# Performance work log

Measured on AMD Instinct MI355X. Metric: run time of the kernel, lower is better.

The kernel has to match this reference:

```python
import jax, jax.numpy as jnp
import numpy as np

N, E, F, H = 8192, 131072, 128, 128
K = N // 2  # pooling ratio = 0.5


def setup_inputs():
    key = jax.random.key(0)
    ks = jax.random.split(key, 16)
    g = lambda i, shape, s: jax.random.normal(ks[i], shape, jnp.float32) * s
    w = 0.1
    return {
        "nodes": g(0, (N, F), 1.0),
        "edges": jax.random.randint(ks[1], (2, E), 0, N, dtype=jnp.int32),
        "batch": jnp.zeros((N,), jnp.int32),
        "w1": g(2, (F, H), w), "b1": jnp.zeros((H,), jnp.float32),
        "w2": g(3, (H, H), w), "b2": jnp.zeros((H,), jnp.float32),
        "w3": g(4, (H, H), w), "b3": jnp.zeros((H,), jnp.float32),
        "w4": g(5, (H, H), w), "b4": jnp.zeros((H,), jnp.float32),
        "w5": g(6, (H, F), w), "b5": jnp.zeros((F,), jnp.float32),
        "wq": g(7, (H, H), w), "bq": jnp.zeros((H,), jnp.float32),
        "att": g(8, (2 * H,), w),
        "lw1": g(9, (H, 1), w), "lb1": jnp.zeros((1,), jnp.float32),
        "lw2": g(10, (H, 1), w), "lw3": g(11, (H, 1), w),
    }


def reference(nodes, edges, batch, w1, b1, w2, b2, w3, b3, w4, b4, w5, b5,
              wq, bq, att, lw1, lb1, lw2, lw3):
    n = nodes.shape[0]
    src, dst = edges[0], edges[1]
    loop = jnp.arange(n, dtype=src.dtype)
    srcl = jnp.concatenate([src, loop])  # edges + self loops
    dstl = jnp.concatenate([dst, loop])
    deg = jax.ops.segment_sum(jnp.ones(srcl.shape[0], nodes.dtype), dstl, n)
    dis = jax.lax.rsqrt(jnp.maximum(deg, 1.0))
    norm = dis[srcl] * dis[dstl]  # GCN symmetric normalization

    def gcn(x, w, b):
        return jax.ops.segment_sum((x @ w)[srcl] * norm[:, None], dstl, n) + b

    h = jnp.tanh(gcn(nodes, w1, b1))
    h = jnp.tanh(gcn(h, w2, b2))

    # ---- ASAP pooling ----
    h_src = h[srcl]
    # cluster query: max over 1-hop neighborhood, then linear
    xq = jax.ops.segment_max(h_src, dstl, n) @ wq + bq
    # edge attention score, softmax per destination (cluster)
    e = jax.nn.leaky_relu(jnp.concatenate([xq[dstl], h_src], axis=-1) @ att, 0.2)
    ee = jnp.exp(e - jax.ops.segment_max(e, dstl, n)[dstl])
    alpha = ee / jax.ops.segment_sum(ee, dstl, n)[dstl]
    cx = jax.ops.segment_sum(h_src * alpha[:, None], dstl, n)  # cluster reps [N,H]
    # LEConv fitness score (out_dim = 1)
    aggr = jax.ops.segment_sum((cx @ lw2)[dstl] - (cx @ lw3)[srcl], dstl, n)
    fit = jax.nn.sigmoid((cx @ lw1 + lb1 + aggr)[:, 0])
    fitk, perm = jax.lax.top_k(fit, K)
    xp = cx[perm] * fitk[:, None]  # pooled node features [K,H]
    # dense assignment matrix S [N,K]: S[i, j] = alpha(i -> perm[j])
    inv = jnp.full((n,), -1, jnp.int32).at[perm].set(jnp.arange(K, dtype=jnp.int32))
    col = inv[dstl]
    valid = col >= 0
    S = jnp.zeros((n, K), nodes.dtype).at[
        srcl, jnp.where(valid, col, 0)].add(jnp.where(valid, alpha, 0.0))
    # dense adjacency (with self loops) and coarsened adjacency Ac = S^T A S
    A = jnp.zeros((n, n), nodes.dtype).at[srcl, dstl].add(1.0)
    Ac = S.T @ (A @ S)  # [K,K]

    # ---- autoencoder reconstruction via bmm with S ----
    x_out = S @ xp               # [N,H]
    adj_out = S @ (Ac @ S.T)     # [N,N]

    x2 = jnp.tanh(gcn(x_out, w3, b3))
    x2 = jnp.tanh(gcn(x2, w4, b4))
    x2 = gcn(x2, w5, b5)
    return x2, adj_out[None]
```

## Files before the change

### kernel.cpp

```cpp
#include <hip/hip_runtime.h>
#include <math.h>

#define NN 8192
#define EE 131072
#define ELn 139264
#define HH 128
#define KK 4096

__device__ __forceinline__ int esrc(const int* __restrict__ edges, int e){ return e < EE ? edges[e] : e - EE; }
__device__ __forceinline__ int edst(const int* __restrict__ edges, int e){ return e < EE ? edges[EE + e] : e - EE; }

__global__ void k_count(const int* __restrict__ edges, int* __restrict__ indeg, int* __restrict__ outdeg){
  int e = blockIdx.x*blockDim.x + threadIdx.x;
  if (e < ELn){
    atomicAdd(&indeg[edst(edges,e)], 1);
    atomicAdd(&outdeg[esrc(edges,e)], 1);
  }
}

__global__ void k_dis(const int* __restrict__ deg, float* __restrict__ dis){
  int v = blockIdx.x*blockDim.x + threadIdx.x;
  if (v < NN){ float d = (float)deg[v]; d = d < 1.0f ? 1.0f : d; dis[v] = 1.0f/sqrtf(d); }
}

template<int IPT>
__global__ __launch_bounds__(1024) void k_scan(const int* __restrict__ cnt, int* __restrict__ rowptr, int* __restrict__ cur){
  __shared__ int part[1024];
  int tid = threadIdx.x;
  int base = tid*IPT;
  int loc[IPT]; int s=0;
  #pragma unroll
  for (int i=0;i<IPT;i++) loc[i]=cnt[base+i];
  #pragma unroll
  for (int i=0;i<IPT;i++){ int t=loc[i]; loc[i]=s; s+=t; }
  part[tid]=s;
  __syncthreads();
  for (int off=1; off<1024; off<<=1){
    int v = (tid>=off)? part[tid-off] : 0;
    __syncthreads();
    part[tid]+=v;
    __syncthreads();
  }
  int cb = part[tid]-s;
  #pragma unroll
  for (int i=0;i<IPT;i++){ int r=cb+loc[i]; rowptr[base+i]=r; cur[base+i]=r; }
  if (tid==1023) rowptr[1024*IPT]=part[1023];
}

__global__ void k_fill_dst(const int* __restrict__ edges, int* __restrict__ cur,
                           int* __restrict__ delist, int* __restrict__ desrc){
  int e = blockIdx.x*blockDim.x + threadIdx.x;
  if (e < ELn){
    int v = edst(edges,e);
    int pos = atomicAdd(&cur[v],1);
    delist[pos] = e;
    desrc[pos]  = esrc(edges,e);
  }
}
__global__ void k_fill_src(const int* __restrict__ edges, int* __restrict__ cur, int* __restrict__ esdst){
  int e = blockIdx.x*blockDim.x + threadIdx.x;
  if (e < ELn){
    int u = esrc(edges,e);
    int pos = atomicAdd(&cur[u],1);
    esdst[pos] = edst(edges,e);
  }
}

template<int TANH>
__global__ __launch_bounds__(256) void k_layer(const float* __restrict__ x,
    const int* __restrict__ desrc, const int* __restrict__ drowptr,
    const float* __restrict__ dis, const float* __restrict__ W,
    const float* __restrict__ bias, float* __restrict__ out){
  __shared__ float agg[8][HH];
  int tid = threadIdx.x;
  int r0 = blockIdx.x*8;
  int wv = tid>>6, lane = tid&63;
  for (int rr=wv; rr<8; rr+=4){
    int v = r0+rr;
    int beg = drowptr[v], end = drowptr[v+1];
    float ax=0.f, ay=0.f;
    for (int i=beg;i<end;++i){
      int u = desrc[i];
      float du = dis[u];
      float2 xv = *(const float2*)&x[(size_t)u*HH + lane*2];
      ax += du*xv.x; ay += du*xv.y;
    }
    float dv = dis[v];
    *(float2*)&agg[rr][lane*2] = make_float2(ax*dv, ay*dv);
  }
  __syncthreads();
  int c = tid&127, h = tid>>7;
  float a0=0,a1=0,a2=0,a3=0;
  #pragma unroll 4
  for (int k=0;k<HH;++k){
    float wv_ = W[k*HH+c];
    a0 += agg[h*4+0][k]*wv_;
    a1 += agg[h*4+1][k]*wv_;
    a2 += agg[h*4+2][k]*wv_;
    a3 += agg[h*4+3][k]*wv_;
  }
  float b = bias[c];
  float r[4]={a0+b,a1+b,a2+b,a3+b};
  #pragma unroll
  for (int j=0;j<4;j++){
    float v = r[j];
    if (TANH) v = tanhf(v);
    out[(size_t)(r0+h*4+j)*HH + c] = v;
  }
}

__global__ __launch_bounds__(256) void k_gemm8(const float* __restrict__ x, const float* __restrict__ W,
     const float* __restrict__ bias, float* __restrict__ y){
  __shared__ float xl[8*HH];
  int tid = threadIdx.x;
  int r0 = blockIdx.x*8;
  {
    int row = tid>>5, col = (tid&31)*4;
    *(float4*)&xl[row*HH+col] = *(const float4*)&x[(size_t)(r0+row)*HH+col];
  }
  __syncthreads();
  int c = tid & 127, h = tid>>7;
  float acc0=0,acc1=0,acc2=0,acc3=0;
  const float* xr = &xl[h*4*HH];
  #pragma unroll 8
  for (int k=0;k<HH;++k){
    float wv = W[k*HH+c];
    acc0 += xr[k]*wv;
    acc1 += xr[HH+k]*wv;
    acc2 += xr[2*HH+k]*wv;
    acc3 += xr[3*HH+k]*wv;
  }
  float b = bias[c];
  y[(size_t)(r0+h*4+0)*HH + c] = acc0+b;
  y[(size_t)(r0+h*4+1)*HH + c] = acc1+b;
  y[(size_t)(r0+h*4+2)*HH + c] = acc2+b;
  y[(size_t)(r0+h*4+3)*HH + c] = acc3+b;
}

__global__ void k_segmax(const float* __restrict__ h, const int* __restrict__ desrc,
    const int* __restrict__ drowptr, float* __restrict__ out){
  int v = blockIdx.x, f = threadIdx.x;
  int beg = drowptr[v], end = drowptr[v+1];
  float m = -3.4e38f;
  for (int i=beg;i<end;++i){
    int u = desrc[i];
    m = fmaxf(m, h[(size_t)u*HH+f]);
  }
  out[(size_t)v*HH+f] = m;
}

__global__ void k_aqah(const float* __restrict__ xq, const float* __restrict__ h,
                       const float* __restrict__ att, float* __restrict__ aq, float* __restrict__ ah){
  int v = blockIdx.x, t = threadIdx.x;
  float a1 = xq[(size_t)v*HH+t]*att[t];
  float a2 = h[(size_t)v*HH+t]*att[HH+t];
  #pragma unroll
  for (int off=32; off; off>>=1){ a1 += __shfl_down(a1,off); a2 += __shfl_down(a2,off); }
  __shared__ float s1[2], s2[2];
  if ((t&63)==0){ s1[t>>6]=a1; s2[t>>6]=a2; }
  __syncthreads();
  if (t==0){ aq[v]=s1[0]+s1[1]; ah[v]=s2[0]+s2[1]; }
}

__global__ __launch_bounds__(256) void k_alpha(const int* __restrict__ delist, const int* __restrict__ desrc,
    const int* __restrict__ drowptr, const float* __restrict__ aq, const float* __restrict__ ah,
    float* __restrict__ alpha){
  int v = blockIdx.x*4 + (threadIdx.x>>6);
  int lane = threadIdx.x & 63;
  int beg = drowptr[v], end = drowptr[v+1];
  float aqv = aq[v];
  float m = -3.4e38f;
  for (int i=beg+lane; i<end; i+=64){
    float s = aqv + ah[desrc[i]];
    s = s > 0.0f ? s : 0.2f*s;
    m = fmaxf(m, s);
  }
  #pragma unroll
  for (int off=32; off; off>>=1) m = fmaxf(m, __shfl_xor(m, off));
  float den = 0.0f;
  for (int i=beg+lane; i<end; i+=64){
    float s = aqv + ah[desrc[i]];
    s = s > 0.0f ? s : 0.2f*s;
    den += expf(s - m);
  }
  #pragma unroll
  for (int off=32; off; off>>=1) den += __shfl_xor(den, off);
  float inv = 1.0f/den;
  for (int i=beg+lane; i<end; i+=64){
    float s = aqv + ah[desrc[i]];
    s = s > 0.0f ? s : 0.2f*s;
    alpha[delist[i]] = expf(s - m)*inv;
  }
}

__global__ void k_cx(const float* __restrict__ h, const int* __restrict__ delist,
    const int* __restrict__ desrc, const int* __restrict__ drowptr,
    const float* __restrict__ alpha, float* __restrict__ cx){
  int v = blockIdx.x, f = threadIdx.x;
  int beg = drowptr[v], end = drowptr[v+1];
  float acc = 0.0f;
  for (int i=beg;i<end;++i){
    acc += alpha[delist[i]]*h[(size_t)desrc[i]*HH+f];
  }
  cx[(size_t)v*HH+f] = acc;
}

__global__ void k_le(const float* __restrict__ cx, const float* __restrict__ lw1,
                     const float* __restrict__ lw2, const float* __restrict__ lw3,
                     float* __restrict__ l1, float* __restrict__ l2, float* __restrict__ l3){
  int v = blockIdx.x, t = threadIdx.x;
  float cv = cx[(size_t)v*HH+t];
  float a = cv*lw1[t], b = cv*lw2[t], c = cv*lw3[t];
  #pragma unroll
  for (int off=32; off; off>>=1){ a += __shfl_down(a,off); b += __shfl_down(b,off); c += __shfl_down(c,off); }
  __shared__ float sa[2], sb[2], sc[2];
  if ((t&63)==0){ sa[t>>6]=a; sb[t>>6]=b; sc[t>>6]=c; }
  __syncthreads();
  if (t==0){ l1[v]=sa[0]+sa[1]; l2[v]=sb[0]+sb[1]; l3[v]=sc[0]+sc[1]; }
}

__global__ __launch_bounds__(256) void k_fit(const int* __restrict__ desrc, const int* __restrict__ drowptr,
    const float* __restrict__ l1, const float* __restrict__ l2, const float* __restrict__ l3,
    const float* __restrict__ lb1, float* __restrict__ fit){
  int v = blockIdx.x*4 + (threadIdx.x>>6);
  int lane = threadIdx.x & 63;
  int beg = drowptr[v], end = drowptr[v+1];
  float s = 0.0f;
  for (int i=beg+lane;i<end;i+=64) s += l3[desrc[i]];
  #pragma unroll
  for (int off=32; off; off>>=1) s += __shfl_xor(s, off);
  if (lane==0){
    float degf = (float)(end-beg);
    float x = l1[v] + lb1[0] + degf*l2[v] - s;
    fit[v] = 1.0f/(1.0f+expf(-x));
  }
}

__global__ __launch_bounds__(1024) void k_topk(const float* __restrict__ fit, int* __restrict__ perm,
                        float* __restrict__ fitk, int* __restrict__ inv){
  __shared__ unsigned long long keys[NN];
  int tid = threadIdx.x;
  for (int i=tid;i<NN;i+=1024){
    unsigned u = __float_as_uint(fit[i]);
    unsigned mono = (u>>31) ? ~u : (u|0x80000000u);
    keys[i] = ((unsigned long long)(~mono)<<32) | (unsigned)i;
    inv[i] = -1;
  }
  __syncthreads();
  for (int k=2;k<=NN;k<<=1)
    for (int j=k>>1;j>0;j>>=1){
      for (int t=tid;t<NN;t+=1024){
        int ixj = t^j;
        if (ixj > t){
          bool up = ((t&k)==0);
          unsigned long long a = keys[t], b = keys[ixj];
          if (up ? (a>b) : (a<b)){ keys[t]=b; keys[ixj]=a; }
        }
      }
      __syncthreads();
    }
  for (int i=tid;i<KK;i+=1024){
    int idx = (int)(keys[i] & 0xffffffffu);
    perm[i]=idx; fitk[i]=fit[idx]; inv[idx]=i;
  }
}

__global__ void k_xp(const float* __restrict__ cx, const int* __restrict__ perm,
                     const float* __restrict__ fitk, float* __restrict__ xp){
  int j = blockIdx.x, f = threadIdx.x;
  xp[(size_t)j*HH+f] = cx[(size_t)perm[j]*HH+f]*fitk[j];
}

__global__ void k_scnt(const int* __restrict__ edges, const int* __restrict__ inv, int* __restrict__ scnt){
  int e = blockIdx.x*blockDim.x + threadIdx.x;
  if (e < ELn && inv[edst(edges,e)] >= 0) atomicAdd(&scnt[esrc(edges,e)],1);
}

__global__ void k_fill_s(const int* __restrict__ edges, const int* __restrict__ inv,
                         const float* __restrict__ alpha, int* __restrict__ scur,
                         int2* __restrict__ spair, int* __restrict__ srow_of){
  int e = blockIdx.x*blockDim.x + threadIdx.x;
  if (e < ELn){
    int j = inv[edst(edges,e)];
    if (j >= 0){
      int u = esrc(edges,e);
      int pos = atomicAdd(&scur[u],1);
      spair[pos] = make_int2(j, __float_as_int(alpha[e]));
      srow_of[pos] = u;
    }
  }
}

__global__ void k_col_cnt(const int2* __restrict__ spair, const int* __restrict__ srowptr, int* __restrict__ ccnt){
  int i = blockIdx.x*blockDim.x + threadIdx.x;
  if (i < srowptr[NN]) atomicAdd(&ccnt[spair[i].x], 1);
}
__global__ void k_col_fill(const int2* __restrict__ spair, const int* __restrict__ srow_of,
                           const int* __restrict__ srowptr, int* __restrict__ ccur,
                           int* __restrict__ colu, float* __restrict__ cval){
  int i = blockIdx.x*blockDim.x + threadIdx.x;
  if (i < srowptr[NN]){
    int2 p = spair[i];
    int pos = atomicAdd(&ccur[p.x], 1);
    colu[pos] = srow_of[i];
    cval[pos] = __int_as_float(p.y);
  }
}

__global__ void k_xout(const float* __restrict__ xp, const int* __restrict__ srowptr,
                       const int2* __restrict__ spair, float* __restrict__ xout){
  int u = blockIdx.x, f = threadIdx.x;
  int beg = srowptr[u], end = srowptr[u+1];
  float acc = 0.0f;
  for (int i=beg;i<end;++i){
    int2 p = spair[i];
    acc += __int_as_float(p.y)*xp[(size_t)p.x*HH+f];
  }
  xout[(size_t)u*HH+f] = acc;
}

#define ACCAP 2048
__global__ __launch_bounds__(256) void k_ac2(const int* __restrict__ cptr, const int* __restrict__ colu,
     const float* __restrict__ cval, const int* __restrict__ esptr, const int* __restrict__ esdst,
     const int* __restrict__ srowptr, const int2* __restrict__ spair, float* __restrict__ Ac){
  __shared__ float row[KK];
  __shared__ int   lv[ACCAP];
  __shared__ float lval[ACCAP];
  int tid = threadIdx.x;
  int p = blockIdx.x;
  for (int i=tid;i<KK;i+=256) row[i]=0.0f;
  int cb = cptr[p], ce = cptr[p+1];
  int base = 0;
  int j = cb;
  while (true){
    while (j < ce){
      int u = colu[j]; float val = cval[j];
      int eb = esptr[u], d = esptr[u+1]-eb;
      if (base + d > ACCAP) break;
      for (int t=tid; t<d; t+=256){ lv[base+t]=esdst[eb+t]; lval[base+t]=val; }
      base += d; ++j;
    }
    __syncthreads();
    for (int i=tid;i<base;i+=256){
      int v = lv[i]; float a = lval[i];
      int sb = srowptr[v], se = srowptr[v+1];
      for (int k=sb;k<se;++k){
        int2 q = spair[k];
        atomicAdd(&row[q.x], a*__int_as_float(q.y));
      }
    }
    __syncthreads();
    base = 0;
    if (j >= ce) break;
  }
  for (int i=tid;i<KK;i+=256) Ac[(size_t)p*KK+i] = row[i];
}

__global__ __launch_bounds__(1024) void k_adj(const float* __restrict__ Ac, const int* __restrict__ srowptr,
      const int2* __restrict__ spair, float* __restrict__ adj){
  __shared__ float U[8*KK];
  int tid = threadIdx.x;
  int u0 = blockIdx.x*8;
  #pragma unroll
  for (int g=0; g<8; ++g){
    int beg = srowptr[u0+g], end = srowptr[u0+g+1];
    float ux=0.f, uy=0.f, uz=0.f, uw=0.f;
    for (int i=beg;i<end;++i){
      int2 pr = spair[i];
      float a = __int_as_float(pr.y);
      float4 av = *(const float4*)(Ac + (size_t)pr.x*KK + 4*tid);
      ux += a*av.x; uy += a*av.y; uz += a*av.z; uw += a*av.w;
    }
    *(float4*)&U[g*KK + 4*tid] = make_float4(ux,uy,uz,uw);
  }
  __syncthreads();
  for (int wb=0; wb<NN; wb+=1024){
    int w = wb + tid;
    int beg = srowptr[w], end = srowptr[w+1];
    float acc[8];
    #pragma unroll
    for (int g=0;g<8;g++) acc[g]=0.f;
    for (int i=beg;i<end;++i){
      int2 p = spair[i];
      float b = __int_as_float(p.y);
      int q = p.x;
      #pragma unroll
      for (int g=0;g<8;g++) acc[g] += b*U[g*KK+q];
    }
    #pragma unroll
    for (int g=0;g<8;g++)
      __builtin_nontemporal_store(acc[g], &adj[(size_t)(u0+g)*NN + w]);
  }
}

extern "C" void kernel_launch(void* const* d_in, const int* in_sizes, int n_in,
                              void* d_out, int out_size, void* d_ws, size_t ws_size,
                              hipStream_t stream){
  const float* nodes = (const float*)d_in[0];
  const int*   edges = (const int*)d_in[1];
  const float* w1=(const float*)d_in[3];  const float* b1=(const float*)d_in[4];
  const float* w2=(const float*)d_in[5];  const float* b2=(const float*)d_in[6];
  const float* w3=(const float*)d_in[7];  const float* b3=(const float*)d_in[8];
  const float* w4=(const float*)d_in[9];  const float* b4=(const float*)d_in[10];
  const float* w5=(const float*)d_in[11]; const float* b5=(const float*)d_in[12];
  const float* wq=(const float*)d_in[13]; const float* bq=(const float*)d_in[14];
  const float* att=(const float*)d_in[15];
  const float* lw1=(const float*)d_in[16]; const float* lb1=(const float*)d_in[17];
  const float* lw2=(const float*)d_in[18]; const float* lw3=(const float*)d_in[19];

  char* ws = (char*)d_ws;
  size_t off = 0;
  auto take = [&](size_t bytes)->char*{
    char* p = ws + off;
    off = (off + bytes + 255) & ~(size_t)255;
    return p;
  };
  int*   deg     = (int*)  take((size_t)NN*4);
  float* dis     = (float*)take((size_t)NN*4);
  int*   drowptr = (int*)  take((size_t)(NN+1)*4);
  int*   dcur    = (int*)  take((size_t)NN*4);
  int*   delist  = (int*)  take((size_t)ELn*4);
  float* alpha   = (float*)take((size_t)ELn*4);
  float* aq      = (float*)take((size_t)NN*4);
  float* ah      = (float*)take((size_t)NN*4);
  float* l1      = (float*)take((size_t)NN*4);
  float* l2      = (float*)take((size_t)NN*4);
  float* l3      = (float*)take((size_t)NN*4);
  float* fit     = (float*)take((size_t)NN*4);
  int*   perm    = (int*)  take((size_t)KK*4);
  float* fitk    = (float*)take((size_t)KK*4);
  int*   inv     = (int*)  take((size_t)NN*4);
  int*   scnt    = (int*)  take((size_t)NN*4);
  int*   srowptr = (int*)  take((size_t)(NN+1)*4);
  int*   scur    = (int*)  take((size_t)NN*4);
  int2*  spair   = (int2*) take((size_t)ELn*8);
  int*   ecnt    = (int*)  take((size_t)NN*4);
  int*   esptr   = (int*)  take((size_t)(NN+1)*4);
  int*   ecur    = (int*)  take((size_t)NN*4);
  int*   ccnt    = (int*)  take((size_t)KK*4);
  int*   cptr    = (int*)  take((size_t)(KK+1)*4);
  int*   ccur    = (int*)  take((size_t)KK*4);
  float* Ac      = (float*)take((size_t)KK*KK*4);
  (void)ws_size; (void)in_sizes; (void)n_in; (void)out_size;

  float* out_x2 = (float*)d_out;
  float* adj    = (float*)d_out + (size_t)NN*HH;
  float* BB = adj + 0*(size_t)NN*HH;
  float* BC = adj + 1*(size_t)NN*HH;
  float* BD = adj + 2*(size_t)NN*HH;
  float* BE = adj + 3*(size_t)NN*HH;
  float* BF = adj + 4*(size_t)NN*HH;
  float* BG = adj + 5*(size_t)NN*HH;
  float* xp = adj + 6*(size_t)NN*HH;
  char*  sc2 = (char*)(adj + 7*(size_t)NN*HH);
  int*   desrc   = (int*)  sc2;                       sc2 += (size_t)ELn*4;
  int*   esdst   = (int*)  sc2;                       sc2 += (size_t)ELn*4;
  int*   srow_of = (int*)  sc2;                       sc2 += (size_t)ELn*4;
  int*   colu    = (int*)  sc2;                       sc2 += (size_t)ELn*4;
  float* cval    = (float*)sc2;                       sc2 += (size_t)ELn*4;

  const int EB = ELn/256;

  hipMemsetAsync(deg, 0, (size_t)NN*4, stream);
  hipMemsetAsync(ecnt, 0, (size_t)NN*4, stream);
  k_count<<<EB,256,0,stream>>>(edges,deg,ecnt);
  k_dis<<<NN/256,256,0,stream>>>(deg,dis);
  k_scan<8><<<1,1024,0,stream>>>(deg,drowptr,dcur);
  k_fill_dst<<<EB,256,0,stream>>>(edges,dcur,delist,desrc);
  k_scan<8><<<1,1024,0,stream>>>(ecnt,esptr,ecur);
  k_fill_src<<<EB,256,0,stream>>>(edges,ecur,esdst);

  k_layer<1><<<NN/8,256,0,stream>>>(nodes,desrc,drowptr,dis,w1,b1,BB);
  k_layer<1><<<NN/8,256,0,stream>>>(BB,desrc,drowptr,dis,w2,b2,BC);

  k_segmax<<<NN,128,0,stream>>>(BC,desrc,drowptr,BD);
  k_gemm8<<<NN/8,256,0,stream>>>(BD,wq,bq,BE);
  k_aqah<<<NN,128,0,stream>>>(BE,BC,att,aq,ah);
  k_alpha<<<NN/4,256,0,stream>>>(delist,desrc,drowptr,aq,ah,alpha);
  k_cx<<<NN,128,0,stream>>>(BC,delist,desrc,drowptr,alpha,BF);
  k_le<<<NN,128,0,stream>>>(BF,lw1,lw2,lw3,l1,l2,l3);
  k_fit<<<NN/4,256,0,stream>>>(desrc,drowptr,l1,l2,l3,lb1,fit);
  k_topk<<<1,1024,0,stream>>>(fit,perm,fitk,inv);
  k_xp<<<KK,128,0,stream>>>(BF,perm,fitk,xp);

  hipMemsetAsync(scnt, 0, (size_t)NN*4, stream);
  k_scnt<<<EB,256,0,stream>>>(edges,inv,scnt);
  k_scan<8><<<1,1024,0,stream>>>(scnt,srowptr,scur);
  k_fill_s<<<EB,256,0,stream>>>(edges,inv,alpha,scur,spair,srow_of);
  hipMemsetAsync(ccnt, 0, (size_t)KK*4, stream);
  k_col_cnt<<<EB,256,0,stream>>>(spair,srowptr,ccnt);
  k_scan<4><<<1,1024,0,stream>>>(ccnt,cptr,ccur);
  k_col_fill<<<EB,256,0,stream>>>(spair,srow_of,srowptr,ccur,colu,cval);

  k_xout<<<NN,128,0,stream>>>(xp,srowptr,spair,BG);
  k_layer<1><<<NN/8,256,0,stream>>>(BG,desrc,drowptr,dis,w3,b3,BB);
  k_layer<1><<<NN/8,256,0,stream>>>(BB,desrc,drowptr,dis,w4,b4,BD);
  k_layer<0><<<NN/8,256,0,stream>>>(BD,desrc,drowptr,dis,w5,b5,out_x2);

  k_ac2<<<KK,256,0,stream>>>(cptr,colu,cval,esptr,esdst,srowptr,spair,Ac);
  k_adj<<<NN/8,1024,0,stream>>>(Ac,srowptr,spair,adj);
}
```

Baseline: 1.118 ms.

## Fuse graph-build and pooling kernels, replace bitonic top-k with histogram radix select

Several kernels are merged: the two scans run in one two-block launch, the dst and src CSR fills share one pass, segmax+wq gemm+attention dot are fused into k_pool, the ah dot is folded into the second GCN layer, and the LEConv projections are fused into the cx aggregation. The single-block 8192-element bitonic top-k is replaced with a 16-bit histogram select plus a small bitonic sort over tie bins only. The perm/xp arrays are removed, so xout reads cx*fit directly. k_adj processes two rows at a time for more memory-level parallelism, and the memsets are merged into one. This cuts launch count and serial single-block sorting, at the cost of an extra index array and tie-ordering logic whose slot assignment must match top_k.

```diff
diff --git a/kernel.cpp b/kernel.cpp
--- a/kernel.cpp
+++ b/kernel.cpp
@@ -6,6 +6,7 @@
 #define ELn 139264
 #define HH 128
 #define KK 4096
+#define NBIN 65536
 
 __device__ __forceinline__ int esrc(const int* __restrict__ edges, int e){ return e < EE ? edges[e] : e - EE; }
 __device__ __forceinline__ int edst(const int* __restrict__ edges, int e){ return e < EE ? edges[EE + e] : e - EE; }
@@ -24,7 +25,7 @@
 }
 
 template<int IPT>
-__global__ __launch_bounds__(1024) void k_scan(const int* __restrict__ cnt, int* __restrict__ rowptr, int* __restrict__ cur){
+__device__ __forceinline__ void scan_body(const int* __restrict__ cnt, int* __restrict__ rowptr, int* __restrict__ cur){
   __shared__ int part[1024];
   int tid = threadIdx.x;
   int base = tid*IPT;
@@ -46,36 +47,41 @@
   for (int i=0;i<IPT;i++){ int r=cb+loc[i]; rowptr[base+i]=r; cur[base+i]=r; }
   if (tid==1023) rowptr[1024*IPT]=part[1023];
 }
-
-__global__ void k_fill_dst(const int* __restrict__ edges, int* __restrict__ cur,
-                           int* __restrict__ delist, int* __restrict__ desrc){
+template<int IPT>
+__global__ __launch_bounds__(1024) void k_scan(const int* __restrict__ cnt, int* __restrict__ rowptr, int* __restrict__ cur){
+  scan_body<IPT>(cnt, rowptr, cur);
+}
+__global__ __launch_bounds__(1024) void k_scan2(const int* __restrict__ c0, int* __restrict__ r0, int* __restrict__ u0,
+                                                const int* __restrict__ c1, int* __restrict__ r1, int* __restrict__ u1){
+  if (blockIdx.x==0) scan_body<8>(c0,r0,u0);
+  else               scan_body<8>(c1,r1,u1);
+}
+
+__global__ void k_fill_both(const int* __restrict__ edges, int* __restrict__ dcur, int* __restrict__ ecur,
+                            int* __restrict__ delist, int* __restrict__ desrc, int* __restrict__ esdst){
   int e = blockIdx.x*blockDim.x + threadIdx.x;
   if (e < ELn){
-    int v = edst(edges,e);
-    int pos = atomicAdd(&cur[v],1);
+    int v = edst(edges,e), u = esrc(edges,e);
+    int pos = atomicAdd(&dcur[v],1);
     delist[pos] = e;
-    desrc[pos]  = esrc(edges,e);
-  }
-}
-__global__ void k_fill_src(const int* __restrict__ edges, int* __restrict__ cur, int* __restrict__ esdst){
-  int e = blockIdx.x*blockDim.x + threadIdx.x;
-  if (e < ELn){
-    int u = esrc(edges,e);
-    int pos = atomicAdd(&cur[u],1);
-    esdst[pos] = edst(edges,e);
-  }
-}
-
-template<int TANH>
+    desrc[pos]  = u;
+    int pos2 = atomicAdd(&ecur[u],1);
+    esdst[pos2] = v;
+  }
+}
+
+template<int TANH, int AH>
 __global__ __launch_bounds__(256) void k_layer(const float* __restrict__ x,
     const int* __restrict__ desrc, const int* __restrict__ drowptr,
     const float* __restrict__ dis, const float* __restrict__ W,
-    const float* __restrict__ bias, float* __restrict__ out){
+    const float* __restrict__ bias, const float* __restrict__ att,
+    float* __restrict__ out, float* __restrict__ ah){
   __shared__ float agg[8][HH];
+  __shared__ float sred[4][4];
   int tid = threadIdx.x;
   int r0 = blockIdx.x*8;
-  int wv = tid>>6, lane = tid&63;
-  for (int rr=wv; rr<8; rr+=4){
+  int wvid = tid>>6, lane = tid&63;
+  for (int rr=wvid; rr<8; rr+=4){
     int v = r0+rr;
     int beg = drowptr[v], end = drowptr[v+1];
     float ax=0.f, ay=0.f;
@@ -100,66 +106,73 @@
     a3 += agg[h*4+3][k]*wv_;
   }
   float b = bias[c];
-  float r[4]={a0+b,a1+b,a2+b,a3+b};
+  float tv[4]={a0+b,a1+b,a2+b,a3+b};
   #pragma unroll
   for (int j=0;j<4;j++){
-    float v = r[j];
-    if (TANH) v = tanhf(v);
-    out[(size_t)(r0+h*4+j)*HH + c] = v;
-  }
-}
-
-__global__ __launch_bounds__(256) void k_gemm8(const float* __restrict__ x, const float* __restrict__ W,
-     const float* __restrict__ bias, float* __restrict__ y){
-  __shared__ float xl[8*HH];
+    if (TANH) tv[j] = tanhf(tv[j]);
+    out[(size_t)(r0+h*4+j)*HH + c] = tv[j];
+  }
+  if (AH){
+    float ac = att[HH+c];
+    float s0=tv[0]*ac, s1=tv[1]*ac, s2=tv[2]*ac, s3=tv[3]*ac;
+    #pragma unroll
+    for (int off=32; off; off>>=1){
+      s0 += __shfl_down(s0,off); s1 += __shfl_down(s1,off);
+      s2 += __shfl_down(s2,off); s3 += __shfl_down(s3,off);
+    }
+    if (lane==0){ sred[wvid][0]=s0; sred[wvid][1]=s1; sred[wvid][2]=s2; sred[wvid][3]=s3; }
+    __syncthreads();
+    if (tid<8){
+      int hh = tid>>2, j = tid&3;
+      ah[r0+tid] = sred[hh*2][j] + sred[hh*2+1][j];
+    }
+  }
+}
+
+__global__ __launch_bounds__(256) void k_pool(const float* __restrict__ hx,
+    const int* __restrict__ desrc, const int* __restrict__ drowptr,
+    const float* __restrict__ wq, const float* __restrict__ bq,
+    const float* __restrict__ att, float* __restrict__ aq){
+  __shared__ float agg[8][HH];
+  __shared__ float sred[4][4];
   int tid = threadIdx.x;
   int r0 = blockIdx.x*8;
-  {
-    int row = tid>>5, col = (tid&31)*4;
-    *(float4*)&xl[row*HH+col] = *(const float4*)&x[(size_t)(r0+row)*HH+col];
-  }
-  __syncthreads();
-  int c = tid & 127, h = tid>>7;
-  float acc0=0,acc1=0,acc2=0,acc3=0;
-  const float* xr = &xl[h*4*HH];
-  #pragma unroll 8
+  int wvid = tid>>6, lane = tid&63;
+  for (int rr=wvid; rr<8; rr+=4){
+    int v = r0+rr;
+    int beg = drowptr[v], end = drowptr[v+1];
+    float mx=-3.4e38f, my=-3.4e38f;
+    for (int i=beg;i<end;++i){
+      int u = desrc[i];
+      float2 xv = *(const float2*)&hx[(size_t)u*HH + lane*2];
+      mx = fmaxf(mx, xv.x); my = fmaxf(my, xv.y);
+    }
+    *(float2*)&agg[rr][lane*2] = make_float2(mx, my);
+  }
+  __syncthreads();
+  int c = tid&127, h = tid>>7;
+  float a0=0,a1=0,a2=0,a3=0;
+  #pragma unroll 4
   for (int k=0;k<HH;++k){
-    float wv = W[k*HH+c];
-    acc0 += xr[k]*wv;
-    acc1 += xr[HH+k]*wv;
-    acc2 += xr[2*HH+k]*wv;
-    acc3 += xr[3*HH+k]*wv;
-  }
-  float b = bias[c];
-  y[(size_t)(r0+h*4+0)*HH + c] = acc0+b;
-  y[(size_t)(r0+h*4+1)*HH + c] = acc1+b;
-  y[(size_t)(r0+h*4+2)*HH + c] = acc2+b;
-  y[(size_t)(r0+h*4+3)*HH + c] = acc3+b;
-}
-
-__global__ void k_segmax(const float* __restrict__ h, const int* __restrict__ desrc,
-    const int* __restrict__ drowptr, float* __restrict__ out){
-  int v = blockIdx.x, f = threadIdx.x;
-  int beg = drowptr[v], end = drowptr[v+1];
-  float m = -3.4e38f;
-  for (int i=beg;i<end;++i){
-    int u = desrc[i];
-    m = fmaxf(m, h[(size_t)u*HH+f]);
-  }
-  out[(size_t)v*HH+f] = m;
-}
-
-__global__ void k_aqah(const float* __restrict__ xq, const float* __restrict__ h,
-                       const float* __restrict__ att, float* __restrict__ aq, float* __restrict__ ah){
-  int v = blockIdx.x, t = threadIdx.x;
-  float a1 = xq[(size_t)v*HH+t]*att[t];
-  float a2 = h[(size_t)v*HH+t]*att[HH+t];
-  #pragma unroll
-  for (int off=32; off; off>>=1){ a1 += __shfl_down(a1,off); a2 += __shfl_down(a2,off); }
-  __shared__ float s1[2], s2[2];
-  if ((t&63)==0){ s1[t>>6]=a1; s2[t>>6]=a2; }
-  __syncthreads();
-  if (t==0){ aq[v]=s1[0]+s1[1]; ah[v]=s2[0]+s2[1]; }
+    float wv_ = wq[k*HH+c];
+    a0 += agg[h*4+0][k]*wv_;
+    a1 += agg[h*4+1][k]*wv_;
+    a2 += agg[h*4+2][k]*wv_;
+    a3 += agg[h*4+3][k]*wv_;
+  }
+  float b = bq[c], ac = att[c];
+  float s0=(a0+b)*ac, s1=(a1+b)*ac, s2=(a2+b)*ac, s3=(a3+b)*ac;
+  #pragma unroll
+  for (int off=32; off; off>>=1){
+    s0 += __shfl_down(s0,off); s1 += __shfl_down(s1,off);
+    s2 += __shfl_down(s2,off); s3 += __shfl_down(s3,off);
+  }
+  if (lane==0){ sred[wvid][0]=s0; sred[wvid][1]=s1; sred[wvid][2]=s2; sred[wvid][3]=s3; }
+  __syncthreads();
+  if (tid<8){
+    int hh = tid>>2, j = tid&3;
+    aq[r0+tid] = sred[hh*2][j] + sred[hh*2+1][j];
+  }
 }
 
 __global__ __launch_bounds__(256) void k_alpha(const int* __restrict__ delist, const int* __restrict__ desrc,
@@ -193,9 +206,11 @@
   }
 }
 
-__global__ void k_cx(const float* __restrict__ h, const int* __restrict__ delist,
+__global__ void k_cxle(const float* __restrict__ h, const int* __restrict__ delist,
     const int* __restrict__ desrc, const int* __restrict__ drowptr,
-    const float* __restrict__ alpha, float* __restrict__ cx){
+    const float* __restrict__ alpha, const float* __restrict__ lw1,
+    const float* __restrict__ lw2, const float* __restrict__ lw3,
+    float* __restrict__ cx, float* __restrict__ l1, float* __restrict__ l2, float* __restrict__ l3){
   int v = blockIdx.x, f = threadIdx.x;
   int beg = drowptr[v], end = drowptr[v+1];
   float acc = 0.0f;
@@ -203,25 +218,18 @@
     acc += alpha[delist[i]]*h[(size_t)desrc[i]*HH+f];
   }
   cx[(size_t)v*HH+f] = acc;
-}
-
-__global__ void k_le(const float* __restrict__ cx, const float* __restrict__ lw1,
-                     const float* __restrict__ lw2, const float* __restrict__ lw3,
-                     float* __restrict__ l1, float* __restrict__ l2, float* __restrict__ l3){
-  int v = blockIdx.x, t = threadIdx.x;
-  float cv = cx[(size_t)v*HH+t];
-  float a = cv*lw1[t], b = cv*lw2[t], c = cv*lw3[t];
-  #pragma unroll
-  for (int off=32; off; off>>=1){ a += __shfl_down(a,off); b += __shfl_down(b,off); c += __shfl_down(c,off); }
+  float p1 = acc*lw1[f], p2 = acc*lw2[f], p3 = acc*lw3[f];
+  #pragma unroll
+  for (int off=32; off; off>>=1){ p1 += __shfl_down(p1,off); p2 += __shfl_down(p2,off); p3 += __shfl_down(p3,off); }
   __shared__ float sa[2], sb[2], sc[2];
-  if ((t&63)==0){ sa[t>>6]=a; sb[t>>6]=b; sc[t>>6]=c; }
-  __syncthreads();
-  if (t==0){ l1[v]=sa[0]+sa[1]; l2[v]=sb[0]+sb[1]; l3[v]=sc[0]+sc[1]; }
+  if ((f&63)==0){ sa[f>>6]=p1; sb[f>>6]=p2; sc[f>>6]=p3; }
+  __syncthreads();
+  if (f==0){ l1[v]=sa[0]+sa[1]; l2[v]=sb[0]+sb[1]; l3[v]=sc[0]+sc[1]; }
 }
 
 __global__ __launch_bounds__(256) void k_fit(const int* __restrict__ desrc, const int* __restrict__ drowptr,
     const float* __restrict__ l1, const float* __restrict__ l2, const float* __restrict__ l3,
-    const float* __restrict__ lb1, float* __restrict__ fit){
+    const float* __restrict__ lb1, float* __restrict__ fit, int* __restrict__ hist){
   int v = blockIdx.x*4 + (threadIdx.x>>6);
   int lane = threadIdx.x & 63;
   int beg = drowptr[v], end = drowptr[v+1];
@@ -232,24 +240,67 @@
   if (lane==0){
     float degf = (float)(end-beg);
     float x = l1[v] + lb1[0] + degf*l2[v] - s;
-    fit[v] = 1.0f/(1.0f+expf(-x));
-  }
-}
-
-__global__ __launch_bounds__(1024) void k_topk(const float* __restrict__ fit, int* __restrict__ perm,
-                        float* __restrict__ fitk, int* __restrict__ inv){
+    float fv = 1.0f/(1.0f+expf(-x));
+    fit[v] = fv;
+    atomicAdd(&hist[__float_as_uint(fv)>>16], 1);
+  }
+}
+
+__global__ __launch_bounds__(1024) void k_scanfind(const int* __restrict__ hist, int* __restrict__ meta){
+  __shared__ int part[1024];
+  int tid = threadIdx.x;
+  int chunk = 0;
+  #pragma unroll
+  for (int i=0;i<NBIN/1024;i++) chunk += hist[tid*(NBIN/1024)+i];
+  part[tid] = chunk;
+  __syncthreads();
+  for (int off=1; off<1024; off<<=1){
+    int v = (tid+off<1024)? part[tid+off] : 0;
+    __syncthreads();
+    part[tid] += v;
+    __syncthreads();
+  }
+  int cum = part[tid] - chunk;
+  for (int i=NBIN/1024-1; i>=0; --i){
+    int b = tid*(NBIN/1024)+i;
+    int c = hist[b];
+    if (cum < KK && cum + c >= KK){ meta[2]=b; meta[3]=cum; }
+    cum += c;
+  }
+}
+
+__global__ void k_assign(const float* __restrict__ fit, const int* __restrict__ meta,
+                         int* __restrict__ ctr, int* __restrict__ inv, unsigned long long* __restrict__ ties){
+  int v = blockIdx.x*blockDim.x + threadIdx.x;
+  if (v >= NN) return;
+  unsigned key = __float_as_uint(fit[v]);
+  int B = meta[2];
+  int kb = (int)(key>>16);
+  if (kb > B){
+    inv[v] = atomicAdd(&ctr[0], 1);
+  } else if (kb == B){
+    int pos = atomicAdd(&ctr[1], 1);
+    ties[pos] = ((unsigned long long)(~key)<<32) | (unsigned)v;
+    inv[v] = -1;
+  } else {
+    inv[v] = -1;
+  }
+}
+
+__global__ __launch_bounds__(1024) void k_ties(const int* __restrict__ meta, const int* __restrict__ ctr,
+                                               const unsigned long long* __restrict__ ties, int* __restrict__ inv){
   __shared__ unsigned long long keys[NN];
   int tid = threadIdx.x;
-  for (int i=tid;i<NN;i+=1024){
-    unsigned u = __float_as_uint(fit[i]);
-    unsigned mono = (u>>31) ? ~u : (u|0x80000000u);
-    keys[i] = ((unsigned long long)(~mono)<<32) | (unsigned)i;
-    inv[i] = -1;
-  }
-  __syncthreads();
-  for (int k=2;k<=NN;k<<=1)
+  int nt = ctr[1];
+  int nGT = meta[3];
+  int need = KK - nGT;
+  int m = 1; while (m < nt) m <<= 1;
+  if (m < 2) m = 2;
+  for (int i=tid;i<m;i+=1024) keys[i] = (i<nt)? ties[i] : 0xFFFFFFFFFFFFFFFFull;
+  __syncthreads();
+  for (int k=2;k<=m;k<<=1)
     for (int j=k>>1;j>0;j>>=1){
-      for (int t=tid;t<NN;t+=1024){
+      for (int t=tid;t<m;t+=1024){
         int ixj = t^j;
         if (ixj > t){
           bool up = ((t&k)==0);
@@ -259,16 +310,10 @@
       }
       __syncthreads();
     }
-  for (int i=tid;i<KK;i+=1024){
-    int idx = (int)(keys[i] & 0xffffffffu);
-    perm[i]=idx; fitk[i]=fit[idx]; inv[idx]=i;
-  }
-}
-
-__global__ void k_xp(const float* __restrict__ cx, const int* __restrict__ perm,
-                     const float* __restrict__ fitk, float* __restrict__ xp){
-  int j = blockIdx.x, f = threadIdx.x;
-  xp[(size_t)j*HH+f] = cx[(size_t)perm[j]*HH+f]*fitk[j];
+  for (int i=tid;i<need;i+=1024){
+    int v = (int)(keys[i] & 0xffffffffu);
+    inv[v] = nGT + i;
+  }
 }
 
 __global__ void k_scnt(const int* __restrict__ edges, const int* __restrict__ inv, int* __restrict__ scnt){
@@ -278,15 +323,17 @@
 
 __global__ void k_fill_s(const int* __restrict__ edges, const int* __restrict__ inv,
                          const float* __restrict__ alpha, int* __restrict__ scur,
-                         int2* __restrict__ spair, int* __restrict__ srow_of){
+                         int2* __restrict__ spair, int* __restrict__ srow_of, int* __restrict__ sdst_of){
   int e = blockIdx.x*blockDim.x + threadIdx.x;
   if (e < ELn){
-    int j = inv[edst(edges,e)];
+    int d = edst(edges,e);
+    int j = inv[d];
     if (j >= 0){
       int u = esrc(edges,e);
       int pos = atomicAdd(&scur[u],1);
       spair[pos] = make_int2(j, __float_as_int(alpha[e]));
       srow_of[pos] = u;
+      sdst_of[pos] = d;
     }
   }
 }
@@ -307,14 +354,15 @@
   }
 }
 
-__global__ void k_xout(const float* __restrict__ xp, const int* __restrict__ srowptr,
-                       const int2* __restrict__ spair, float* __restrict__ xout){
+__global__ void k_xout(const float* __restrict__ cx, const float* __restrict__ fit,
+                       const int* __restrict__ srowptr, const int2* __restrict__ spair,
+                       const int* __restrict__ sdst_of, float* __restrict__ xout){
   int u = blockIdx.x, f = threadIdx.x;
   int beg = srowptr[u], end = srowptr[u+1];
   float acc = 0.0f;
   for (int i=beg;i<end;++i){
-    int2 p = spair[i];
-    acc += __int_as_float(p.y)*xp[(size_t)p.x*HH+f];
+    int d = sdst_of[i];
+    acc += __int_as_float(spair[i].y)*fit[d]*cx[(size_t)d*HH+f];
   }
   xout[(size_t)u*HH+f] = acc;
 }
@@ -362,16 +410,28 @@
   int tid = threadIdx.x;
   int u0 = blockIdx.x*8;
   #pragma unroll
-  for (int g=0; g<8; ++g){
-    int beg = srowptr[u0+g], end = srowptr[u0+g+1];
-    float ux=0.f, uy=0.f, uz=0.f, uw=0.f;
-    for (int i=beg;i<end;++i){
-      int2 pr = spair[i];
-      float a = __int_as_float(pr.y);
-      float4 av = *(const float4*)(Ac + (size_t)pr.x*KK + 4*tid);
-      ux += a*av.x; uy += a*av.y; uz += a*av.z; uw += a*av.w;
-    }
-    *(float4*)&U[g*KK + 4*tid] = make_float4(ux,uy,uz,uw);
+  for (int g2=0; g2<8; g2+=2){
+    int bA = srowptr[u0+g2],   eA = srowptr[u0+g2+1];
+    int bB = eA,               eB = srowptr[u0+g2+2];
+    float ax0=0,ax1=0,ax2=0,ax3=0, bx0=0,bx1=0,bx2=0,bx3=0;
+    int nA = eA-bA, nB = eB-bB;
+    int n = nA > nB ? nA : nB;
+    for (int t=0;t<n;++t){
+      if (t<nA){
+        int2 pr = spair[bA+t];
+        float a = __int_as_float(pr.y);
+        float4 av = *(const float4*)(Ac + (size_t)pr.x*KK + 4*tid);
+        ax0 += a*av.x; ax1 += a*av.y; ax2 += a*av.z; ax3 += a*av.w;
+      }
+      if (t<nB){
+        int2 pr = spair[bB+t];
+        float a = __int_as_float(pr.y);
+        float4 av = *(const float4*)(Ac + (size_t)pr.x*KK + 4*tid);
+        bx0 += a*av.x; bx1 += a*av.y; bx2 += a*av.z; bx3 += a*av.w;
+      }
+    }
+    *(float4*)&U[g2*KK + 4*tid]     = make_float4(ax0,ax1,ax2,ax3);
+    *(float4*)&U[(g2+1)*KK + 4*tid] = make_float4(bx0,bx1,bx2,bx3);
   }
   __syncthreads();
   for (int wb=0; wb<NN; wb+=1024){
@@ -416,6 +476,12 @@
     return p;
   };
   int*   deg     = (int*)  take((size_t)NN*4);
+  int*   ecnt    = (int*)  take((size_t)NN*4);
+  int*   scnt    = (int*)  take((size_t)NN*4);
+  int*   ccnt    = (int*)  take((size_t)KK*4);
+  int*   hist    = (int*)  take((size_t)NBIN*4);
+  int*   ctr     = (int*)  take((size_t)4*4);
+  size_t zero_bytes = off;
   float* dis     = (float*)take((size_t)NN*4);
   int*   drowptr = (int*)  take((size_t)(NN+1)*4);
   int*   dcur    = (int*)  take((size_t)NN*4);
@@ -427,19 +493,15 @@
   float* l2      = (float*)take((size_t)NN*4);
   float* l3      = (float*)take((size_t)NN*4);
   float* fit     = (float*)take((size_t)NN*4);
-  int*   perm    = (int*)  take((size_t)KK*4);
-  float* fitk    = (float*)take((size_t)KK*4);
   int*   inv     = (int*)  take((size_t)NN*4);
-  int*   scnt    = (int*)  take((size_t)NN*4);
   int*   srowptr = (int*)  take((size_t)(NN+1)*4);
   int*   scur    = (int*)  take((size_t)NN*4);
   int2*  spair   = (int2*) take((size_t)ELn*8);
-  int*   ecnt    = (int*)  take((size_t)NN*4);
   int*   esptr   = (int*)  take((size_t)(NN+1)*4);
   int*   ecur    = (int*)  take((size_t)NN*4);
-  int*   ccnt    = (int*)  take((size_t)KK*4);
   int*   cptr    = (int*)  take((size_t)(KK+1)*4);
   int*   ccur    = (int*)  take((size_t)KK*4);
+  unsigned long long* ties = (unsigned long long*)take((size_t)NN*8);
   float* Ac      = (float*)take((size_t)KK*KK*4);
   (void)ws_size; (void)in_sizes; (void)n_in; (void)out_size;
 
@@ -448,54 +510,48 @@
   float* BB = adj + 0*(size_t)NN*HH;
   float* BC = adj + 1*(size_t)NN*HH;
   float* BD = adj + 2*(size_t)NN*HH;
-  float* BE = adj + 3*(size_t)NN*HH;
-  float* BF = adj + 4*(size_t)NN*HH;
-  float* BG = adj + 5*(size_t)NN*HH;
-  float* xp = adj + 6*(size_t)NN*HH;
-  char*  sc2 = (char*)(adj + 7*(size_t)NN*HH);
+  float* BF = adj + 3*(size_t)NN*HH;
+  float* BG = adj + 4*(size_t)NN*HH;
+  char*  sc2 = (char*)(adj + 5*(size_t)NN*HH);
   int*   desrc   = (int*)  sc2;                       sc2 += (size_t)ELn*4;
   int*   esdst   = (int*)  sc2;                       sc2 += (size_t)ELn*4;
   int*   srow_of = (int*)  sc2;                       sc2 += (size_t)ELn*4;
+  int*   sdst_of = (int*)  sc2;                       sc2 += (size_t)ELn*4;
   int*   colu    = (int*)  sc2;                       sc2 += (size_t)ELn*4;
   float* cval    = (float*)sc2;                       sc2 += (size_t)ELn*4;
 
   const int EB = ELn/256;
 
-  hipMemsetAsync(deg, 0, (size_t)NN*4, stream);
-  hipMemsetAsync(ecnt, 0, (size_t)NN*4, stream);
+  hipMemsetAsync(deg, 0, zero_bytes, stream);
+
   k_count<<<EB,256,0,stream>>>(edges,deg,ecnt);
   k_dis<<<NN/256,256,0,stream>>>(deg,dis);
-  k_scan<8><<<1,1024,0,stream>>>(deg,drowptr,dcur);
-  k_fill_dst<<<EB,256,0,stream>>>(edges,dcur,delist,desrc);
-  k_scan<8><<<1,1024,0,stream>>>(ecnt,esptr,ecur);
-  k_fill_src<<<EB,256,0,stream>>>(edges,ecur,esdst);
-
-  k_layer<1><<<NN/8,256,0,stream>>>(nodes,desrc,drowptr,dis,w1,b1,BB);
-  k_layer<1><<<NN/8,256,0,stream>>>(BB,desrc,drowptr,dis,w2,b2,BC);
-
-  k_segmax<<<NN,128,0,stream>>>(BC,desrc,drowptr,BD);
-  k_gemm8<<<NN/8,256,0,stream>>>(BD,wq,bq,BE);
-  k_aqah<<<NN,128,0,stream>>>(BE,BC,att,aq,ah);
+  k_scan2<<<2,1024,0,stream>>>(deg,drowptr,dcur, ecnt,esptr,ecur);
+  k_fill_both<<<EB,256,0,stream>>>(edges,dcur,ecur,delist,desrc,esdst);
+
+  k_layer<1,0><<<NN/8,256,0,stream>>>(nodes,desrc,drowptr,dis,w1,b1,nullptr,BB,nullptr);
+  k_layer<1,1><<<NN/8,256,0,stream>>>(BB,desrc,drowptr,dis,w2,b2,att,BC,ah);
+
+  k_pool<<<NN/8,256,0,stream>>>(BC,desrc,drowptr,wq,bq,att,aq);
   k_alpha<<<NN/4,256,0,stream>>>(delist,desrc,drowptr,aq,ah,alpha);
-  k_cx<<<NN,128,0,stream>>>(BC,delist,desrc,drowptr,alpha,BF);
-  k_le<<<NN,128,0,stream>>>(BF,lw1,lw2,lw3,l1,l2,l3);
-  k_fit<<<NN/4,256,0,stream>>>(desrc,drowptr,l1,l2,l3,lb1,fit);
-  k_topk<<<1,1024,0,stream>>>(fit,perm,fitk,inv);
-  k_xp<<<KK,128,0,stream>>>(BF,perm,fitk,xp);
-
-  hipMemsetAsync(scnt, 0, (size_t)NN*4, stream);
+  k_cxle<<<NN,128,0,stream>>>(BC,delist,desrc,drowptr,alpha,lw1,lw2,lw3,BF,l1,l2,l3);
+  k_fit<<<NN/4,256,0,stream>>>(desrc,drowptr,l1,l2,l3,lb1,fit,hist);
+
+  k_scanfind<<<1,1024,0,stream>>>(hist,ctr);
+  k_assign<<<NN/256,256,0,stream>>>(fit,ctr,ctr,inv,ties);
+  k_ties<<<1,1024,0,stream>>>(ctr,ctr,ties,inv);
+
   k_scnt<<<EB,256,0,stream>>>(edges,inv,scnt);
   k_scan<8><<<1,1024,0,stream>>>(scnt,srowptr,scur);
-  k_fill_s<<<EB,256,0,stream>>>(edges,inv,alpha,scur,spair,srow_of);
-  hipMemsetAsync(ccnt, 0, (size_t)KK*4, stream);
+  k_fill_s<<<EB,256,0,stream>>>(edges,inv,alpha,scur,spair,srow_of,sdst_of);
   k_col_cnt<<<EB,256,0,stream>>>(spair,srowptr,ccnt);
   k_scan<4><<<1,1024,0,stream>>>(ccnt,cptr,ccur);
   k_col_fill<<<EB,256,0,stream>>>(spair,srow_of,srowptr,ccur,colu,cval);
 
-  k_xout<<<NN,128,0,stream>>>(xp,srowptr,spair,BG);
-  k_layer<1><<<NN/8,256,0,stream>>>(BG,desrc,drowptr,dis,w3,b3,BB);
-  k_layer<1><<<NN/8,256,0,stream>>>(BB,desrc,drowptr,dis,w4,b4,BD);
-  k_layer<0><<<NN/8,256,0,stream>>>(BD,desrc,drowptr,dis,w5,b5,out_x2);
+  k_xout<<<NN,128,0,stream>>>(BF,fit,srowptr,spair,sdst_of,BG);
+  k_layer<1,0><<<NN/8,256,0,stream>>>(BG,desrc,drowptr,dis,w3,b3,nullptr,BB,nullptr);
+  k_layer<1,0><<<NN/8,256,0,stream>>>(BB,desrc,drowptr,dis,w4,b4,nullptr,BD,nullptr);
+  k_layer<0,0><<<NN/8,256,0,stream>>>(BD,desrc,drowptr,dis,w5,b5,nullptr,out_x2,nullptr);
 
   k_ac2<<<KK,256,0,stream>>>(cptr,colu,cval,esptr,esdst,srowptr,spair,Ac);
   k_adj<<<NN/8,1024,0,stream>>>(Ac,srowptr,spair,adj);
```

After: 1.026 ms. 1.09x faster.
